# Performance work log

Hardware: AMD Instinct MI355X
Metric: run time of the kernel (lower is better)

The kernel has to match this reference:

```python
import jax, jax.numpy as jnp
import numpy as np

N = 8192
IN_F = 128
OUT_F = 128


def setup_inputs() -> dict:
    key = jax.random.key(0)
    k1, k2, k3, k4 = jax.random.split(key, 4)
    h = jax.random.normal(k1, (N, IN_F), dtype=jnp.float32)
    pos = jax.random.normal(k2, (N, 1, 3), dtype=jnp.float32)
    # xavier_uniform-ish scale for params
    W = jax.random.uniform(k3, (IN_F, OUT_F), dtype=jnp.float32,
                           minval=-1.0, maxval=1.0) * (1.414 * np.sqrt(6.0 / (IN_F + OUT_F)))
    a = jax.random.uniform(k4, (2 * OUT_F + 3, 1), dtype=jnp.float32,
                           minval=-1.0, maxval=1.0) * (1.414 * np.sqrt(6.0 / (2 * OUT_F + 3 + 1)))
    return {"h": h, "pos": pos, "W": W, "a": a}


def reference(h, pos, W, a):
    # Wh: [N, F]
    Wh = h @ W
    F_ = Wh.shape[1]
    a1 = a[:F_, 0]          # weights on Wh[j] (the repeated / neighbor features)
    a2 = a[F_:2 * F_, 0]    # weights on Wh[i] (the repeat_interleaved / center features)
    a3 = a[2 * F_:, 0]      # weights on pos[i] - pos[j]
    p = pos.reshape(-1, 3)  # [N, 3]
    s_j = Wh @ a1           # [N]
    s_i = Wh @ a2           # [N]
    p_a = p @ a3            # [N]
    # e[i, j] = leaky_relu(Wh[j].a1 + Wh[i].a2 + (pos[i]-pos[j]).a3)
    e = jax.nn.leaky_relu(s_i[:, None] + s_j[None, :] + p_a[:, None] - p_a[None, :],
                          negative_slope=0.2)  # [N, N]
    attention = jax.nn.softmax(e, axis=1)
    # eval mode: dropout is identity
    h_prime = attention @ Wh  # [N, F]
    return jax.nn.elu(h_prime)
```

## Files before the change

kernel.cpp:

```cpp
#include <hip/hip_runtime.h>
#include <hip/hip_bf16.h>

#define N 8192
#define F 128
#define JC 16
#define JSLICE (N / JC)
#define CHUNKJ 32
#define NSC (JSLICE / CHUNKJ)

typedef __attribute__((ext_vector_type(4)))  float f32x4;
typedef __attribute__((ext_vector_type(16))) float f32x16;
typedef __attribute__((ext_vector_type(8)))  short short8;

static __device__ __forceinline__ short bf16bits(float x) {
  __hip_bfloat16 b = __float2bfloat16(x);
  return *reinterpret_cast<short*>(&b);
}

static __device__ __forceinline__ void gload_lds16(const void* g, void* lds) {
  __builtin_amdgcn_global_load_lds(
      (const __attribute__((address_space(1))) void*)g,
      (__attribute__((address_space(3))) void*)lds, 16, 0, 0);
}

__global__ __launch_bounds__(256) void k_gemm_cd(
    const float* __restrict__ h, const float* __restrict__ pos,
    const float* __restrict__ W, const float* __restrict__ a,
    unsigned short* __restrict__ WhTf, float* __restrict__ cArr,
    float* __restrict__ dArr)
{
  __shared__ float Ws[128 * 128];
  const int tid = threadIdx.x;
  const int r0  = blockIdx.x * 16;

  {
    f32x4* Ws4 = (f32x4*)Ws;
    const f32x4* Wg4 = (const f32x4*)W;
#pragma unroll
    for (int q = 0; q < 16; ++q) Ws4[q * 256 + tid] = Wg4[q * 256 + tid];
  }
  __syncthreads();

  const int rg  = tid >> 5;
  const int c32 = tid & 31;

  f32x4 acc0, acc1;
#pragma unroll
  for (int i = 0; i < 4; ++i) { acc0[i] = 0.0f; acc1[i] = 0.0f; }

  const f32x4* h40 = (const f32x4*)(h + (size_t)(r0 + rg * 2) * 128);
  const f32x4* h41 = (const f32x4*)(h + (size_t)(r0 + rg * 2 + 1) * 128);
  const f32x4* Ws4 = (const f32x4*)Ws;

#pragma unroll 4
  for (int k4 = 0; k4 < 32; ++k4) {
    f32x4 hv0 = h40[k4];
    f32x4 hv1 = h41[k4];
#pragma unroll
    for (int e = 0; e < 4; ++e) {
      f32x4 w = Ws4[(k4 * 4 + e) * 32 + c32];
      acc0 += hv0[e] * w;
      acc1 += hv1[e] * w;
    }
  }

  f32x4 a1v = *(const f32x4*)(a + c32 * 4);
  f32x4 a2v = *(const f32x4*)(a + 128 + c32 * 4);
#pragma unroll
  for (int rr = 0; rr < 2; ++rr) {
    f32x4 accR = rr ? acc1 : acc0;
    f32x4 t1 = accR * a1v;
    f32x4 t2 = accR * a2v;
    float s1 = t1[0] + t1[1] + t1[2] + t1[3];
    float s2 = t2[0] + t2[1] + t2[2] + t2[3];
#pragma unroll
    for (int m = 1; m < 32; m <<= 1) {
      s1 += __shfl_xor(s1, m);
      s2 += __shfl_xor(s2, m);
    }
    if (c32 == 0) {
      const int row = r0 + rg * 2 + rr;
      float pa = pos[row * 3 + 0] * a[256] + pos[row * 3 + 1] * a[257] +
                 pos[row * 3 + 2] * a[258];
      cArr[row] = s2 + pa;
      dArr[row] = s1 - pa;
    }
  }

  __syncthreads();
  float* tmp = Ws;
  {
    const int base = (rg * 2) * 132 + c32 * 4;
    *(f32x4*)&tmp[base]       = acc0;
    *(f32x4*)&tmp[base + 132] = acc1;
  }
  __syncthreads();
  {
    const int col  = tid >> 1;
    const int half = tid & 1;
    short8 o;
#pragma unroll
    for (int rr = 0; rr < 8; ++rr)
      o[rr] = bf16bits(tmp[(half * 8 + rr) * 132 + col]);
    *(short8*)(WhTf + (size_t)(r0 >> 4) * 2048 + col * 16 + half * 8) = o;
  }
}

__global__ __launch_bounds__(256, 4) void k_flash(
    const unsigned short* __restrict__ WhTf, const float* __restrict__ cArr,
    const float* __restrict__ dArr, float* __restrict__ pnum,
    float* __restrict__ pden)
{
  __shared__ __align__(16) unsigned short bufS[2][CHUNKJ * 128];
  __shared__ __align__(16) float dS[JSLICE];

  const int tid = threadIdx.x;
  const int rb  = blockIdx.x & 63;
  const int jc  = blockIdx.x >> 6;
  const int r0  = rb * 128;

  const int w  = tid >> 6;
  const int l  = tid & 63;
  const int cl = l & 31;
  const int kh = l >> 5;

  const unsigned short* gBase = WhTf + ((size_t)jc * 32) * 2048;

  {
    const char* gs = (const char*)gBase + (w * 2) * 1024 + l * 16;
    char* ld = (char*)&bufS[0][0] + (w * 2) * 1024;
    gload_lds16(gs, ld);
    gload_lds16(gs + 1024, ld + 1024);
    if (tid < JSLICE / 4)
      ((f32x4*)dS)[tid] = ((const f32x4*)(dArr + (size_t)jc * JSLICE))[tid];
  }
  __syncthreads();

  const float L2E = 1.44269504f;
  const float ci = cArr[r0 + w * 32 + cl] * L2E;

  f32x16 acc0, acc1, acc2, acc3;
#pragma unroll
  for (int i = 0; i < 16; ++i) { acc0[i] = 0; acc1[i] = 0; acc2[i] = 0; acc3[i] = 0; }
  float denA = 0.0f, denB = 0.0f;

  for (int sc = 0; sc < NSC; ++sc) {
    const int cur = sc & 1;
    if (sc + 1 < NSC) {
      const char* gs = (const char*)gBase + (size_t)(sc + 1) * (CHUNKJ * 128 * 2)
                     + (w * 2) * 1024 + l * 16;
      char* ld = (char*)&bufS[cur ^ 1][0] + (w * 2) * 1024;
      gload_lds16(gs, ld);
      gload_lds16(gs + 1024, ld + 1024);
    }

#pragma unroll
    for (int ks = 0; ks < 2; ++ks) {
      const unsigned short* bs = &bufS[cur][ks * 2048];
      short8 b0 = *(const short8*)(bs +    0 + cl * 16 + kh * 8);
      short8 b1 = *(const short8*)(bs +  512 + cl * 16 + kh * 8);
      short8 b2 = *(const short8*)(bs + 1024 + cl * 16 + kh * 8);
      short8 b3 = *(const short8*)(bs + 1536 + cl * 16 + kh * 8);

      const int jo = sc * CHUNKJ + ks * 16 + kh * 8;
      f32x4 dj0 = *(const f32x4*)&dS[jo];
      f32x4 dj1 = *(const f32x4*)&dS[jo + 4];

      short8 af;
#pragma unroll
      for (int e = 0; e < 8; ++e) {
        float dj = (e < 4) ? dj0[e] : dj1[e - 4];
        float u = __builtin_fmaf(dj, L2E, ci);
        u = fmaxf(u, 0.2f * u);
        float pv = __builtin_amdgcn_exp2f(u);
        if (e & 1) denB += pv; else denA += pv;
        af[e] = bf16bits(pv);
      }

      acc0 = __builtin_amdgcn_mfma_f32_32x32x16_bf16(af, b0, acc0, 0, 0, 0);
      acc1 = __builtin_amdgcn_mfma_f32_32x32x16_bf16(af, b1, acc1, 0, 0, 0);
      acc2 = __builtin_amdgcn_mfma_f32_32x32x16_bf16(af, b2, acc2, 0, 0, 0);
      acc3 = __builtin_amdgcn_mfma_f32_32x32x16_bf16(af, b3, acc3, 0, 0, 0);
    }
    __syncthreads();
  }

  float den = denA + denB;
  den += __shfl_xor(den, 32);

  {
    float* base = pnum + (size_t)jc * N * F + (size_t)(r0 + w * 32) * 128;
#pragma unroll
    for (int reg = 0; reg < 16; ++reg) {
      const int row = (reg & 3) + 8 * (reg >> 2) + 4 * kh;
      float* rp = base + row * 128 + cl;
      rp[0]  = acc0[reg];
      rp[32] = acc1[reg];
      rp[64] = acc2[reg];
      rp[96] = acc3[reg];
    }
    if (l < 32) pden[(size_t)jc * N + r0 + w * 32 + l] = den;
  }
}

__global__ __launch_bounds__(256) void k_final(
    const float* __restrict__ pnum, const float* __restrict__ pden,
    float* __restrict__ out)
{
  const int g = blockIdx.x * 256 + threadIdx.x;
  const int row = g >> 5;
  f32x4 n;
#pragma unroll
  for (int i = 0; i < 4; ++i) n[i] = 0.0f;
  float dd = 0.0f;
#pragma unroll
  for (int c = 0; c < JC; ++c) {
    n += ((const f32x4*)pnum)[(size_t)c * (N * F / 4) + g];
    dd += pden[(size_t)c * N + row];
  }
  f32x4 r = n * (1.0f / dd);
#pragma unroll
  for (int i = 0; i < 4; ++i) {
    float x = r[i];
    r[i] = x > 0.0f ? x : (__builtin_amdgcn_exp2f(x * 1.44269504f) - 1.0f);
  }
  ((f32x4*)out)[g] = r;
}

extern "C" void kernel_launch(void* const* d_in, const int* in_sizes, int n_in,
                              void* d_out, int out_size, void* d_ws, size_t ws_size,
                              hipStream_t stream)
{
  const float* h   = (const float*)d_in[0];
  const float* pos = (const float*)d_in[1];
  const float* W   = (const float*)d_in[2];
  const float* a   = (const float*)d_in[3];
  float* out = (float*)d_out;

  char* ws = (char*)d_ws;
  unsigned short* WhTf = (unsigned short*)ws;
  float* cArr = (float*)(ws + (size_t)2 * 1024 * 1024);
  float* dArr = cArr + N;
  float* pden = dArr + N;
  float* pnum = pden + (size_t)JC * N;

  hipLaunchKernelGGL(k_gemm_cd, dim3(512), dim3(256), 0, stream,
                     h, pos, W, a, WhTf, cArr, dArr);
  hipLaunchKernelGGL(k_flash, dim3(64 * JC), dim3(256), 0, stream,
                     WhTf, cArr, dArr, pnum, pden);
  hipLaunchKernelGGL(k_final, dim3((N * F / 4) / 256), dim3(256), 0, stream,
                     pnum, pden, out);
}
```

Baseline: 109.6 us.

## Load attention B-tiles directly from global into registers, dropping LDS staging

The flash kernel no longer stages WhTf chunks through a double-buffered LDS buffer with global_load_lds and per-chunk barriers. Each wave now reads its B fragments straight from global memory into registers, prefetching one 16-column step ahead, and the loop body handles a single step. This removes the block-wide barriers and the LDS traffic. In exchange, all four waves of a block fetch the same data separately through the caches, and the shallow register prefetch may leave global load latency exposed. The final prefetch reads just past the slice, which stays inside the workspace.

```diff
diff --git a/kernel.cpp b/kernel.cpp
--- a/kernel.cpp
+++ b/kernel.cpp
@@ -5,8 +5,6 @@
 #define F 128
 #define JC 16
 #define JSLICE (N / JC)
-#define CHUNKJ 32
-#define NSC (JSLICE / CHUNKJ)
 
 typedef __attribute__((ext_vector_type(4)))  float f32x4;
 typedef __attribute__((ext_vector_type(16))) float f32x16;
@@ -15,12 +13,6 @@
 static __device__ __forceinline__ short bf16bits(float x) {
   __hip_bfloat16 b = __float2bfloat16(x);
   return *reinterpret_cast<short*>(&b);
-}
-
-static __device__ __forceinline__ void gload_lds16(const void* g, void* lds) {
-  __builtin_amdgcn_global_load_lds(
-      (const __attribute__((address_space(1))) void*)g,
-      (__attribute__((address_space(3))) void*)lds, 16, 0, 0);
 }
 
 __global__ __launch_bounds__(256) void k_gemm_cd(
@@ -111,7 +103,6 @@
     const float* __restrict__ dArr, float* __restrict__ pnum,
     float* __restrict__ pden)
 {
-  __shared__ __align__(16) unsigned short bufS[2][CHUNKJ * 128];
   __shared__ __align__(16) float dS[JSLICE];
 
   const int tid = threadIdx.x;
@@ -124,16 +115,8 @@
   const int cl = l & 31;
   const int kh = l >> 5;
 
-  const unsigned short* gBase = WhTf + ((size_t)jc * 32) * 2048;
-
-  {
-    const char* gs = (const char*)gBase + (w * 2) * 1024 + l * 16;
-    char* ld = (char*)&bufS[0][0] + (w * 2) * 1024;
-    gload_lds16(gs, ld);
-    gload_lds16(gs + 1024, ld + 1024);
-    if (tid < JSLICE / 4)
-      ((f32x4*)dS)[tid] = ((const f32x4*)(dArr + (size_t)jc * JSLICE))[tid];
-  }
+  if (tid < JSLICE / 4)
+    ((f32x4*)dS)[tid] = ((const f32x4*)(dArr + (size_t)jc * JSLICE))[tid];
   __syncthreads();
 
   const float L2E = 1.44269504f;
@@ -144,45 +127,44 @@
   for (int i = 0; i < 16; ++i) { acc0[i] = 0; acc1[i] = 0; acc2[i] = 0; acc3[i] = 0; }
   float denA = 0.0f, denB = 0.0f;
 
-  for (int sc = 0; sc < NSC; ++sc) {
-    const int cur = sc & 1;
-    if (sc + 1 < NSC) {
-      const char* gs = (const char*)gBase + (size_t)(sc + 1) * (CHUNKJ * 128 * 2)
-                     + (w * 2) * 1024 + l * 16;
-      char* ld = (char*)&bufS[cur ^ 1][0] + (w * 2) * 1024;
-      gload_lds16(gs, ld);
-      gload_lds16(gs + 1024, ld + 1024);
-    }
-
-#pragma unroll
-    for (int ks = 0; ks < 2; ++ks) {
-      const unsigned short* bs = &bufS[cur][ks * 2048];
-      short8 b0 = *(const short8*)(bs +    0 + cl * 16 + kh * 8);
-      short8 b1 = *(const short8*)(bs +  512 + cl * 16 + kh * 8);
-      short8 b2 = *(const short8*)(bs + 1024 + cl * 16 + kh * 8);
-      short8 b3 = *(const short8*)(bs + 1536 + cl * 16 + kh * 8);
-
-      const int jo = sc * CHUNKJ + ks * 16 + kh * 8;
-      f32x4 dj0 = *(const f32x4*)&dS[jo];
-      f32x4 dj1 = *(const f32x4*)&dS[jo + 4];
-
-      short8 af;
-#pragma unroll
-      for (int e = 0; e < 8; ++e) {
-        float dj = (e < 4) ? dj0[e] : dj1[e - 4];
-        float u = __builtin_fmaf(dj, L2E, ci);
-        u = fmaxf(u, 0.2f * u);
-        float pv = __builtin_amdgcn_exp2f(u);
-        if (e & 1) denB += pv; else denA += pv;
-        af[e] = bf16bits(pv);
-      }
-
-      acc0 = __builtin_amdgcn_mfma_f32_32x32x16_bf16(af, b0, acc0, 0, 0, 0);
-      acc1 = __builtin_amdgcn_mfma_f32_32x32x16_bf16(af, b1, acc1, 0, 0, 0);
-      acc2 = __builtin_amdgcn_mfma_f32_32x32x16_bf16(af, b2, acc2, 0, 0, 0);
-      acc3 = __builtin_amdgcn_mfma_f32_32x32x16_bf16(af, b3, acc3, 0, 0, 0);
-    }
-    __syncthreads();
+  const unsigned short* bPtr =
+      WhTf + (size_t)(jc * (JSLICE / 16)) * 2048 + cl * 16 + kh * 8;
+  const float* dPtr = dS + kh * 8;
+
+  short8 b0 = *(const short8*)(bPtr);
+  short8 b1 = *(const short8*)(bPtr + 512);
+  short8 b2 = *(const short8*)(bPtr + 1024);
+  short8 b3 = *(const short8*)(bPtr + 1536);
+  bPtr += 2048;
+
+  const int iters = JSLICE / 16;
+  for (int s = 0; s < iters; ++s) {
+    short8 n0 = *(const short8*)(bPtr);
+    short8 n1 = *(const short8*)(bPtr + 512);
+    short8 n2 = *(const short8*)(bPtr + 1024);
+    short8 n3 = *(const short8*)(bPtr + 1536);
+
+    f32x4 dj0 = *(const f32x4*)(dPtr);
+    f32x4 dj1 = *(const f32x4*)(dPtr + 4);
+
+    short8 af;
+#pragma unroll
+    for (int e = 0; e < 8; ++e) {
+      float dj = (e < 4) ? dj0[e] : dj1[e - 4];
+      float u = __builtin_fmaf(dj, L2E, ci);
+      u = fmaxf(u, 0.2f * u);
+      float pv = __builtin_amdgcn_exp2f(u);
+      if (e & 1) denB += pv; else denA += pv;
+      af[e] = bf16bits(pv);
+    }
+
+    acc0 = __builtin_amdgcn_mfma_f32_32x32x16_bf16(af, b0, acc0, 0, 0, 0);
+    acc1 = __builtin_amdgcn_mfma_f32_32x32x16_bf16(af, b1, acc1, 0, 0, 0);
+    acc2 = __builtin_amdgcn_mfma_f32_32x32x16_bf16(af, b2, acc2, 0, 0, 0);
+    acc3 = __builtin_amdgcn_mfma_f32_32x32x16_bf16(af, b3, acc3, 0, 0, 0);
+
+    b0 = n0; b1 = n1; b2 = n2; b3 = n3;
+    bPtr += 2048; dPtr += 16;
   }
 
   float den = denA + denB;
```

New measurement: 111.2 us. About the same (+1.5%).
